# Kernel optimization log

Measured on AMD Instinct MI355X. Metric: run time of the kernel, lower is better.

The kernel has to match this reference:

```python
import jax, jax.numpy as jnp
import numpy as np

B, S, D = 4, 2048, 1024
H, N = 8, 16
HN = H * N
L = 2
DFF = 4 * D
V = 32000
C = 1024


def layer_norm(x, g, b, eps=1e-5):
    m = jnp.mean(x, axis=-1, keepdims=True)
    v = jnp.mean(jnp.square(x - m), axis=-1, keepdims=True)
    return (x - m) * jax.lax.rsqrt(v + eps) * g + b


def ssm_scan(alpha, b):
    # alpha, b: [B, S, H, N]; h_t = alpha_t * h_{t-1} + b_t
    h0 = jnp.zeros((alpha.shape[0], alpha.shape[2], alpha.shape[3]), alpha.dtype)

    def step(h, ab):
        a_t, b_t = ab
        h = a_t * h + b_t
        return h, h

    _, hs = jax.lax.scan(step, h0, (jnp.swapaxes(alpha, 0, 1), jnp.swapaxes(b, 0, 1)))
    return jnp.swapaxes(hs, 0, 1)  # [B, S, H, N]


def setup_inputs() -> dict:
    key = jax.random.key(0)
    ks = jax.random.split(key, 30)

    def rn(k, shape, std):
        return (jax.random.normal(k, shape, jnp.float32) * std).astype(jnp.float32)

    xav_d_hn = float(np.sqrt(6.0 / (D + HN)))
    xav_hn_d = float(np.sqrt(6.0 / (HN + D)))
    xav_d_ff = float(np.sqrt(6.0 / (D + DFF)))
    xav_ff_d = float(np.sqrt(6.0 / (DFF + D)))

    inp = {
        "x": jax.random.randint(ks[0], (B, S), 0, V),
        "emb": rn(ks[1], (V, D), 0.02),
        "pos_emb": rn(ks[2], (S, D), 0.02),
        # SSM layers (stacked over L). Weights stored [in, out].
        "alpha_W": rn(ks[3], (L, D, HN), 0.01),
        "alpha_b": jnp.full((L, HN), 2.0, jnp.float32),
        "in_W": jax.random.uniform(ks[4], (L, D, HN), jnp.float32, -xav_d_hn, xav_d_hn),
        "in_b": jnp.zeros((L, HN), jnp.float32),
        "out_W": jax.random.uniform(ks[5], (L, HN, D), jnp.float32, -xav_hn_d, xav_hn_d),
        "out_b": jnp.zeros((L, D), jnp.float32),
        "ssm_g": jnp.ones((L, D), jnp.float32),
        "ssm_beta": jnp.zeros((L, D), jnp.float32),
        # SwiGLU layers
        "w1_W": jax.random.uniform(ks[6], (L, D, DFF), jnp.float32, -xav_d_ff, xav_d_ff),
        "w1_b": jnp.zeros((L, DFF), jnp.float32),
        "w2_W": jax.random.uniform(ks[7], (L, DFF, D), jnp.float32, -xav_ff_d, xav_ff_d),
        "w2_b": jnp.zeros((L, D), jnp.float32),
        "w3_W": jax.random.uniform(ks[8], (L, D, DFF), jnp.float32, -xav_d_ff, xav_d_ff),
        "w3_b": jnp.zeros((L, DFF), jnp.float32),
        "ff_g": jnp.ones((L, D), jnp.float32),
        "ff_beta": jnp.zeros((L, D), jnp.float32),
        # output norm + head
        "on_g": jnp.ones((D,), jnp.float32),
        "on_beta": jnp.zeros((D,), jnp.float32),
        "h1_W": rn(ks[9], (D, 2 * D), 0.02),
        "h1_b": jnp.zeros((2 * D,), jnp.float32),
        "h2_W": rn(ks[10], (2 * D, C), 0.02),
        "h2_b": jnp.zeros((C,), jnp.float32),
    }
    return inp


def reference(x, emb, pos_emb, alpha_W, alpha_b, in_W, in_b, out_W, out_b,
              ssm_g, ssm_beta, w1_W, w1_b, w2_W, w2_b, w3_W, w3_b,
              ff_g, ff_beta, on_g, on_beta, h1_W, h1_b, h2_W, h2_b):
    b, s = x.shape
    h = emb[x] + pos_emb[:s][None, :, :]  # [B,S,D]
    for l in range(L):
        # DiagonalSSMLayer (dropout eval -> identity)
        xn = layer_norm(h, ssm_g[l], ssm_beta[l])
        alpha = jax.nn.sigmoid(xn @ alpha_W[l] + alpha_b[l]).reshape(b, s, H, N)
        bb = (xn @ in_W[l] + in_b[l]).reshape(b, s, H, N)
        hs = ssm_scan(alpha, bb).reshape(b, s, HN)
        h = h + hs @ out_W[l] + out_b[l]
        # SwiGLU block
        xn = layer_norm(h, ff_g[l], ff_beta[l])
        h = h + (jax.nn.silu(xn @ w1_W[l] + w1_b[l]) * (xn @ w3_W[l] + w3_b[l])) @ w2_W[l] + w2_b[l]
    h = layer_norm(h, on_g, on_beta)
    logits = jax.nn.gelu(h @ h1_W + h1_b, approximate=False) @ h2_W + h2_b
    return logits  # [B, S, C]
```

## Files before the change

kernel.cpp:

```cpp
#include <hip/hip_runtime.h>
#include <hip/hip_bf16.h>
#include <math.h>

#define B_    4
#define S_    2048
#define D_    1024
#define H_    8
#define N_    16
#define HN_   128
#define L_    2
#define DFF_  4096
#define C_    1024
#define MTOK  8192

using bf16 = __hip_bfloat16;
typedef __attribute__((ext_vector_type(8))) short  short8;
typedef __attribute__((ext_vector_type(4))) float  f32x4;

static __device__ __forceinline__ float sigmoidf_(float x) { return 1.f / (1.f + expf(-x)); }

static __device__ __forceinline__ unsigned short f2bf_bits(float f) {
    bf16 h = __float2bfloat16(f);
    return __builtin_bit_cast(unsigned short, h);
}

#define GLOAD_LDS(gp, lp) \
    __builtin_amdgcn_global_load_lds((__attribute__((address_space(1))) void*)(gp), \
                                     (__attribute__((address_space(3))) void*)(lp), 16, 0, 0)

#define VMCNT(n) asm volatile("s_waitcnt vmcnt(" #n ")" ::: "memory")
#define BARRIER() do { asm volatile("" ::: "memory"); __builtin_amdgcn_s_barrier(); \
                       asm volatile("" ::: "memory"); } while (0)

__global__ __launch_bounds__(256) void transpose_k(const float* __restrict__ src,
                                                   bf16* __restrict__ dst,
                                                   int K, int N, int rstride, int roff) {
    __shared__ float t[32][33];
    int n0 = blockIdx.x * 32, k0 = blockIdx.y * 32;
    int tx = threadIdx.x, ty = threadIdx.y;
    #pragma unroll
    for (int i = ty; i < 32; i += 8)
        t[i][tx] = src[(size_t)(k0 + i) * N + n0 + tx];
    __syncthreads();
    #pragma unroll
    for (int i = ty; i < 32; i += 8)
        dst[((size_t)(n0 + i) * rstride + roff) * K + k0 + tx] = __float2bfloat16(t[tx][i]);
}

__global__ __launch_bounds__(256) void embed_k(const int* __restrict__ x,
                                               const float* __restrict__ emb,
                                               const float* __restrict__ pos,
                                               float* __restrict__ h) {
    int tok = blockIdx.x, t = threadIdx.x;
    int id = x[tok];
    int s  = tok & (S_ - 1);
    float4 a = ((const float4*)(emb + (size_t)id * D_))[t];
    float4 p = ((const float4*)(pos + (size_t)s * D_))[t];
    float4 r; r.x = a.x + p.x; r.y = a.y + p.y; r.z = a.z + p.z; r.w = a.w + p.w;
    ((float4*)(h + (size_t)tok * D_))[t] = r;
}

__global__ __launch_bounds__(256) void ln_k(const float* __restrict__ x,
                                            const float* __restrict__ g,
                                            const float* __restrict__ be,
                                            bf16* __restrict__ out) {
    int row = blockIdx.x, t = threadIdx.x;
    float4 v = ((const float4*)(x + (size_t)row * D_))[t];
    float s  = v.x + v.y + v.z + v.w;
    float sq = v.x * v.x + v.y * v.y + v.z * v.z + v.w * v.w;
    #pragma unroll
    for (int o = 32; o > 0; o >>= 1) {
        s  += __shfl_down(s, o);
        sq += __shfl_down(sq, o);
    }
    __shared__ float red[8];
    __shared__ float mv[2];
    int wave = t >> 6, lane = t & 63;
    if (lane == 0) { red[wave] = s; red[4 + wave] = sq; }
    __syncthreads();
    if (t == 0) {
        float S0 = red[0] + red[1] + red[2] + red[3];
        float Q  = red[4] + red[5] + red[6] + red[7];
        float m  = S0 * (1.f / 1024.f);
        float var = Q * (1.f / 1024.f) - m * m;
        mv[0] = m; mv[1] = rsqrtf(var + 1e-5f);
    }
    __syncthreads();
    float m = mv[0], rs = mv[1];
    float4 gg = ((const float4*)g)[t];
    float4 bb = ((const float4*)be)[t];
    ushort4 o;
    o.x = f2bf_bits((v.x - m) * rs * gg.x + bb.x);
    o.y = f2bf_bits((v.y - m) * rs * gg.y + bb.y);
    o.z = f2bf_bits((v.z - m) * rs * gg.z + bb.z);
    o.w = f2bf_bits((v.w - m) * rs * gg.w + bb.w);
    ((ushort4*)(out + (size_t)row * D_))[t] = o;
}

__global__ __launch_bounds__(256) void ssm_scan_k(const float* __restrict__ ab,
                                                  bf16* __restrict__ hs) {
    const int CL = S_ / 16;
    int bh = blockIdx.x;
    int b = bh >> 3, hh = bh & 7;
    int t = threadIdx.x;
    int chunk = t >> 4, n = t & 15;
    size_t rowbase = (size_t)b * S_ + (size_t)chunk * CL;
    const float* ap = ab + rowbase * 256 + hh * 16 + n;
    const float* bp = ap + 128;

    float A = 1.f, Bc = 0.f;
    for (int i = 0; i < CL; i++) {
        float a = ap[(size_t)i * 256], bv = bp[(size_t)i * 256];
        A *= a; Bc = a * Bc + bv;
    }
    __shared__ float sA[16][16], sB[16][16], sH[16][16];
    sA[chunk][n] = A; sB[chunk][n] = Bc;
    __syncthreads();
    if (t < 16) {
        float run = 0.f;
        #pragma unroll
        for (int c = 0; c < 16; c++) {
            sH[c][t] = run;
            run = sA[c][t] * run + sB[c][t];
        }
    }
    __syncthreads();
    float hrun = sH[chunk][n];
    bf16* op = hs + rowbase * 128 + hh * 16 + n;
    for (int i = 0; i < CL; i++) {
        float a = ap[(size_t)i * 256], bv = bp[(size_t)i * 256];
        hrun = a * hrun + bv;
        op[(size_t)i * 128] = __float2bfloat16(hrun);
    }
}

enum { EP_AB = 0, EP_BIAS_RES = 1, EP_BIAS_BF16 = 2, EP_SILUMUL_BF16 = 3,
       EP_GELU_BF16 = 4, EP_BIAS_F32 = 5, EP_W13 = 6 };

template <int EP>
static __device__ __forceinline__ void ep_store(
    float v, size_t idx, int col,
    float* __restrict__ outF, bf16* __restrict__ outB,
    const float* __restrict__ b1, const float* __restrict__ b2,
    const float* __restrict__ resF, const bf16* __restrict__ resB) {
    if constexpr (EP == EP_AB) {
        if (col < HN_) v = sigmoidf_(v + b1[col]);
        else           v = v + b2[col - HN_];
        outF[idx] = v;
    } else if constexpr (EP == EP_BIAS_RES) {
        outF[idx] = v + b1[col] + resF[idx];
    } else if constexpr (EP == EP_BIAS_BF16) {
        outB[idx] = __float2bfloat16(v + b1[col]);
    } else if constexpr (EP == EP_SILUMUL_BF16) {
        float c1 = __bfloat162float(resB[idx]);
        float sil = c1 * sigmoidf_(c1);
        outB[idx] = __float2bfloat16((v + b1[col]) * sil);
    } else if constexpr (EP == EP_GELU_BF16) {
        float xv = v + b1[col];
        outB[idx] = __float2bfloat16(0.5f * xv * (1.f + erff(xv * 0.70710678118f)));
    } else {
        outF[idx] = v + b1[col];
    }
}

template <int EP>
__global__ __launch_bounds__(256) void gemm_k(
    const bf16* __restrict__ A, const bf16* __restrict__ W,
    float* __restrict__ outF, bf16* __restrict__ outB,
    const float* __restrict__ b1, const float* __restrict__ b2,
    const float* __restrict__ resF, const bf16* __restrict__ resB,
    int M, int N, int K) {
    __shared__ __align__(16) bf16 As[128 * 64];
    __shared__ __align__(16) bf16 Bs[128 * 64];
    const int tid = threadIdx.x;
    const int wave = tid >> 6, lane = tid & 63;
    const int bm = blockIdx.x * 128, bn = blockIdx.y * 128;
    const int wr = (wave >> 1) * 64, wc = (wave & 1) * 64;

    f32x4 acc[4][4];
    #pragma unroll
    for (int m = 0; m < 4; m++)
        #pragma unroll
        for (int n = 0; n < 4; n++) acc[m][n] = f32x4{0.f, 0.f, 0.f, 0.f};

    const int srow = tid >> 3;
    const int skc  = (tid & 7) * 8;

    for (int k0 = 0; k0 < K; k0 += 64) {
        #pragma unroll
        for (int rr = 0; rr < 4; rr++) {
            int row = rr * 32 + srow;
            GLOAD_LDS(A + (size_t)(bm + row) * K + k0 + skc, As + row * 64 + skc);
            GLOAD_LDS(W + (size_t)(bn + row) * K + k0 + skc, Bs + row * 64 + skc);
        }
        __syncthreads();
        #pragma unroll
        for (int ks = 0; ks < 2; ks++) {
            const int kb = ks * 32 + (lane >> 4) * 8;
            short8 af[4], bfr[4];
            #pragma unroll
            for (int m = 0; m < 4; m++)
                af[m] = *reinterpret_cast<const short8*>(As + (wr + m * 16 + (lane & 15)) * 64 + kb);
            #pragma unroll
            for (int n = 0; n < 4; n++)
                bfr[n] = *reinterpret_cast<const short8*>(Bs + (wc + n * 16 + (lane & 15)) * 64 + kb);
            #pragma unroll
            for (int m = 0; m < 4; m++)
                #pragma unroll
                for (int n = 0; n < 4; n++)
                    acc[m][n] = __builtin_amdgcn_mfma_f32_16x16x32_bf16(af[m], bfr[n], acc[m][n], 0, 0, 0);
        }
        __syncthreads();
    }

    const int cb = bn + wc + (lane & 15);
    const int rb = bm + wr + (lane >> 4) * 4;
    #pragma unroll
    for (int m = 0; m < 4; m++)
        #pragma unroll
        for (int n = 0; n < 4; n++) {
            int col = cb + n * 16;
            #pragma unroll
            for (int i = 0; i < 4; i++) {
                int row = rb + m * 16 + i;
                ep_store<EP>(acc[m][n][i], (size_t)row * N + col, col,
                             outF, outB, b1, b2, resF, resB);
            }
        }
}

extern __shared__ __align__(16) char smem_g256[];

template <int BN, int EP>
__global__ __launch_bounds__(512, 2) void gemm256_k(
    const bf16* __restrict__ A, const bf16* __restrict__ W,
    float* __restrict__ outF, bf16* __restrict__ outB,
    const float* __restrict__ b1, const float* __restrict__ b2,
    const float* __restrict__ resF, const bf16* __restrict__ resB,
    int M, int N, int K) {
    constexpr int NR   = BN / 64;
    constexpr int NBJ  = BN / 64;
    constexpr int WCS  = NR * 16;
    constexpr int ASZB = 256 * 64 * 2;
    constexpr int BSZB = BN * 64 * 2;
    constexpr int BUFB = ASZB + BSZB;

    const int tid = threadIdx.x;
    const int wid = tid >> 6, lane = tid & 63;
    const int wr = wid >> 2, wc = wid & 3;
    const int l15 = lane & 15, l4 = lane >> 4;

    const int nwg = gridDim.x;
    const int bid = ((int)blockIdx.x & 7) * (nwg >> 3) + ((int)blockIdx.x >> 3);
    const int gx = M >> 8;
    const int bm = (bid % gx) * 256;
    const int bn = (bid / gx) * BN;

    const int nt = K >> 6;

    const int tr   = tid >> 3;
    const int cc8  = (((tid & 7) ^ (tr & 7)) << 3);
    const bf16* gA0 = A + (size_t)(bm + tr) * K + cc8;
    const bf16* gB0 = W + (size_t)(bn + tr) * K + cc8;
    const int ldsc = tid << 4;

    auto stageA = [&](int t, int j) {
        GLOAD_LDS(gA0 + (size_t)j * ((size_t)K << 6) + ((size_t)t << 6),
                  smem_g256 + (size_t)(t & 1) * BUFB + ldsc + (j << 13));
    };
    auto stageB = [&](int t, int j) {
        GLOAD_LDS(gB0 + (size_t)j * ((size_t)K << 6) + ((size_t)t << 6),
                  smem_g256 + (size_t)(t & 1) * BUFB + ASZB + ldsc + (j << 13));
    };

    const int swz   = (lane & 7) << 4;
    const int kof0  = ((l4 << 4)) ^ swz;
    const int kof1  = (64 + (l4 << 4)) ^ swz;
    const int rbaseA = (wr * 128 + l15) << 7;
    const int rbaseB = ASZB + ((wc * WCS + l15) << 7);

    auto rdA = [&](int bo, int m, int kof) -> short8 {
        return *reinterpret_cast<const short8*>(smem_g256 + bo + rbaseA + (m << 11) + kof);
    };
    auto rdB = [&](int bo, int n, int kof) -> short8 {
        return *reinterpret_cast<const short8*>(smem_g256 + bo + rbaseB + (n << 11) + kof);
    };

    f32x4 acc[8][NR];
    #pragma unroll
    for (int m = 0; m < 8; m++)
        #pragma unroll
        for (int n = 0; n < NR; n++) acc[m][n] = f32x4{0.f, 0.f, 0.f, 0.f};

    #pragma unroll
    for (int j = 0; j < 4; j++) stageA(0, j);
    #pragma unroll
    for (int j = 0; j < NBJ; j++) stageB(0, j);
    #pragma unroll
    for (int j = 0; j < 4; j++) stageA(1, j);
    #pragma unroll
    for (int j = 0; j < NBJ; j++) stageB(1, j);

    short8 a0[4], a1[4], bF0[NR], bF1[NR];

    for (int v = 0; v < nt; ++v) {
        const int bo = (v & 1) * BUFB;
        if (v == 0)            { if constexpr (BN == 256) VMCNT(8); else VMCNT(6); }
        else if (v + 1 < nt)   { if constexpr (BN == 256) VMCNT(6); else VMCNT(4); }
        else                   VMCNT(0);
        BARRIER();

        #pragma unroll
        for (int m = 0; m < 4; m++) a0[m] = rdA(bo, m, kof0);
        #pragma unroll
        for (int n = 0; n < NR; n++) bF0[n] = rdB(bo, n, kof0);
        #pragma unroll
        for (int n = 0; n < NR; n++) bF1[n] = rdB(bo, n, kof1);
        if (v >= 1 && v + 1 < nt) { stageA(v + 1, 1); stageA(v + 1, 3); }
        BARRIER();
        #pragma unroll
        for (int m = 0; m < 4; m++) a1[m] = rdA(bo, m, kof1);
        __builtin_amdgcn_s_setprio(1);
        #pragma unroll
        for (int m = 0; m < 4; m++)
            #pragma unroll
            for (int n = 0; n < NR; n++)
                acc[m][n] = __builtin_amdgcn_mfma_f32_16x16x32_bf16(a0[m], bF0[n], acc[m][n], 0, 0, 0);
        __builtin_amdgcn_s_setprio(0);
        BARRIER();

        #pragma unroll
        for (int m = 0; m < 4; m++) a0[m] = rdA(bo, 4 + m, kof0);
        __builtin_amdgcn_s_setprio(1);
        #pragma unroll
        for (int m = 0; m < 4; m++)
            #pragma unroll
            for (int n = 0; n < NR; n++)
                acc[m][n] = __builtin_amdgcn_mfma_f32_16x16x32_bf16(a1[m], bF1[n], acc[m][n], 0, 0, 0);
        __builtin_amdgcn_s_setprio(0);
        BARRIER();

        if (v + 2 < nt) {
            #pragma unroll
            for (int j = 0; j < NBJ; j++) stageB(v + 2, j);
            stageA(v + 2, 0); stageA(v + 2, 2);
        }
        #pragma unroll
        for (int m = 0; m < 4; m++) a1[m] = rdA(bo, 4 + m, kof1);
        __builtin_amdgcn_s_setprio(1);
        #pragma unroll
        for (int m = 0; m < 4; m++)
            #pragma unroll
            for (int n = 0; n < NR; n++)
                acc[4 + m][n] = __builtin_amdgcn_mfma_f32_16x16x32_bf16(a0[m], bF0[n], acc[4 + m][n], 0, 0, 0);
        __builtin_amdgcn_s_setprio(0);
        BARRIER();

        __builtin_amdgcn_s_setprio(1);
        #pragma unroll
        for (int m = 0; m < 4; m++)
            #pragma unroll
            for (int n = 0; n < NR; n++)
                acc[4 + m][n] = __builtin_amdgcn_mfma_f32_16x16x32_bf16(a1[m], bF1[n], acc[4 + m][n], 0, 0, 0);
        __builtin_amdgcn_s_setprio(0);
        BARRIER();
    }

    const int gc0 = bn + wc * WCS + l15;
    const int gr0 = bm + wr * 128 + l4 * 4;
    #pragma unroll
    for (int m = 0; m < 8; m++)
        #pragma unroll
        for (int n = 0; n < NR; n++) {
            int col = gc0 + n * 16;
            #pragma unroll
            for (int i = 0; i < 4; i++) {
                int row = gr0 + m * 16 + i;
                if constexpr (EP == EP_W13) {
                    float xv = acc[m][n][i] + ((col & 1) ? b2[col >> 1] : b1[col >> 1]);
                    float part = __shfl_xor(xv, 1);
                    if (!(col & 1)) {
                        float r = xv * sigmoidf_(xv) * part;
                        outB[(size_t)row * (N >> 1) + (col >> 1)] = __float2bfloat16(r);
                    }
                } else {
                    ep_store<EP>(acc[m][n][i], (size_t)row * N + col, col,
                                 outF, outB, b1, b2, resF, resB);
                }
            }
        }
}

extern "C" void kernel_launch(void* const* d_in, const int* in_sizes, int n_in,
                              void* d_out, int out_size, void* d_ws, size_t ws_size,
                              hipStream_t stream) {
    const int*   x       = (const int*)  d_in[0];
    const float* emb     = (const float*)d_in[1];
    const float* pos_emb = (const float*)d_in[2];
    const float* alpha_W = (const float*)d_in[3];
    const float* alpha_b = (const float*)d_in[4];
    const float* in_W    = (const float*)d_in[5];
    const float* in_b    = (const float*)d_in[6];
    const float* out_W   = (const float*)d_in[7];
    const float* out_b   = (const float*)d_in[8];
    const float* ssm_g   = (const float*)d_in[9];
    const float* ssm_be  = (const float*)d_in[10];
    const float* w1_W    = (const float*)d_in[11];
    const float* w1_b    = (const float*)d_in[12];
    const float* w2_W    = (const float*)d_in[13];
    const float* w2_b    = (const float*)d_in[14];
    const float* w3_W    = (const float*)d_in[15];
    const float* w3_b    = (const float*)d_in[16];
    const float* ff_g    = (const float*)d_in[17];
    const float* ff_be   = (const float*)d_in[18];
    const float* on_g    = (const float*)d_in[19];
    const float* on_be   = (const float*)d_in[20];
    const float* h1_W    = (const float*)d_in[21];
    const float* h1_b    = (const float*)d_in[22];
    const float* h2_W    = (const float*)d_in[23];
    const float* h2_b    = (const float*)d_in[24];
    float* outp = (float*)d_out;
    (void)in_sizes; (void)n_in; (void)out_size; (void)ws_size;

    hipFuncSetAttribute((const void*)gemm256_k<256, EP_W13>,       hipFuncAttributeMaxDynamicSharedMemorySize, 131072);
    hipFuncSetAttribute((const void*)gemm256_k<256, EP_GELU_BF16>, hipFuncAttributeMaxDynamicSharedMemorySize, 131072);
    hipFuncSetAttribute((const void*)gemm256_k<128, EP_BIAS_RES>,  hipFuncAttributeMaxDynamicSharedMemorySize, 98304);
    hipFuncSetAttribute((const void*)gemm256_k<128, EP_BIAS_F32>,  hipFuncAttributeMaxDynamicSharedMemorySize, 98304);

    char* ws = (char*)d_ws;
    size_t off = 0;
    auto alloc = [&](size_t bytes) { size_t o = off; off += (bytes + 255) & ~(size_t)255; return o; };
    float* h    = (float*)(ws + alloc((size_t)MTOK * D_ * 4));
    bf16*  xn   = (bf16*) (ws + alloc((size_t)MTOK * D_ * 2));
    bf16*  abw  = (bf16*) (ws + alloc((size_t)L_ * 256 * D_ * 2));
    bf16*  outw = (bf16*) (ws + alloc((size_t)L_ * D_ * HN_ * 2));
    bf16*  wfw  = (bf16*) (ws + alloc((size_t)L_ * 2 * DFF_ * D_ * 2));
    bf16*  w2w  = (bf16*) (ws + alloc((size_t)L_ * D_ * DFF_ * 2));
    bf16*  h1w  = (bf16*) (ws + alloc((size_t)2048 * D_ * 2));
    bf16*  h2w  = (bf16*) (ws + alloc((size_t)D_ * 2048 * 2));
    float* ab   = (float*)(ws + alloc((size_t)MTOK * 256 * 4));
    bf16*  hs   = (bf16*) (ws + alloc((size_t)MTOK * HN_ * 2));
    bf16*  c1   = (bf16*) (ws + alloc((size_t)MTOK * DFF_ * 2));

    auto T = [&](const float* src, bf16* dst, int K, int N, int rs, int ro) {
        transpose_k<<<dim3(N / 32, K / 32), dim3(32, 8), 0, stream>>>(src, dst, K, N, rs, ro);
    };

    for (int l = 0; l < L_; l++) {
        T(alpha_W + (size_t)l * D_ * HN_,  abw + (size_t)l * 256 * D_,                    D_,  HN_, 1, 0);
        T(in_W    + (size_t)l * D_ * HN_,  abw + (size_t)l * 256 * D_ + (size_t)HN_ * D_, D_,  HN_, 1, 0);
        T(out_W   + (size_t)l * HN_ * D_,  outw + (size_t)l * D_ * HN_,                   HN_, D_,  1, 0);
        T(w1_W    + (size_t)l * D_ * DFF_, wfw + (size_t)l * 2 * DFF_ * D_,               D_,  DFF_, 2, 0);
        T(w3_W    + (size_t)l * D_ * DFF_, wfw + (size_t)l * 2 * DFF_ * D_,               D_,  DFF_, 2, 1);
        T(w2_W    + (size_t)l * DFF_ * D_, w2w + (size_t)l * D_ * DFF_,                   DFF_, D_, 1, 0);
    }
    T(h1_W, h1w, D_, 2048, 1, 0);
    T(h2_W, h2w, 2048, D_, 1, 0);

    embed_k<<<MTOK, 256, 0, stream>>>(x, emb, pos_emb, h);

    for (int l = 0; l < L_; l++) {
        ln_k<<<MTOK, 256, 0, stream>>>(h, ssm_g + l * D_, ssm_be + l * D_, xn);
        gemm_k<EP_AB><<<dim3(64, 2), 256, 0, stream>>>(
            xn, abw + (size_t)l * 256 * D_, ab, nullptr,
            alpha_b + l * HN_, in_b + l * HN_, nullptr, nullptr, MTOK, 256, D_);
        ssm_scan_k<<<B_ * H_, 256, 0, stream>>>(ab, hs);
        gemm_k<EP_BIAS_RES><<<dim3(64, 8), 256, 0, stream>>>(
            hs, outw + (size_t)l * D_ * HN_, h, nullptr,
            out_b + l * D_, nullptr, h, nullptr, MTOK, D_, HN_);
        ln_k<<<MTOK, 256, 0, stream>>>(h, ff_g + l * D_, ff_be + l * D_, xn);
        gemm256_k<256, EP_W13><<<dim3((MTOK / 256) * (2 * DFF_ / 256)), 512, 131072, stream>>>(
            xn, wfw + (size_t)l * 2 * DFF_ * D_, nullptr, c1,
            w1_b + l * DFF_, w3_b + l * DFF_, nullptr, nullptr, MTOK, 2 * DFF_, D_);
        gemm256_k<128, EP_BIAS_RES><<<dim3((MTOK / 256) * (D_ / 128)), 512, 98304, stream>>>(
            c1, w2w + (size_t)l * D_ * DFF_, h, nullptr,
            w2_b + l * D_, nullptr, h, nullptr, MTOK, D_, DFF_);
    }

    ln_k<<<MTOK, 256, 0, stream>>>(h, on_g, on_be, xn);
    gemm256_k<256, EP_GELU_BF16><<<dim3((MTOK / 256) * (2048 / 256)), 512, 131072, stream>>>(
        xn, h1w, nullptr, c1, h1_b, nullptr, nullptr, nullptr, MTOK, 2048, D_);
    gemm256_k<128, EP_BIAS_F32><<<dim3((MTOK / 256) * (C_ / 128)), 512, 98304, stream>>>(
        c1, h2w, outp, nullptr, h2_b, nullptr, nullptr, nullptr, MTOK, C_, 2048);
}
```

Baseline: 1.178 ms.

## Restructure gemm256 main loop into quadrant phases with split B staging

```diff
diff --git a/kernel.cpp b/kernel.cpp
--- a/kernel.cpp
+++ b/kernel.cpp
@@ -28,7 +28,9 @@
     __builtin_amdgcn_global_load_lds((__attribute__((address_space(1))) void*)(gp), \
                                      (__attribute__((address_space(3))) void*)(lp), 16, 0, 0)
 
-#define VMCNT(n) asm volatile("s_waitcnt vmcnt(" #n ")" ::: "memory")
+#define VMCNT(n)  asm volatile("s_waitcnt vmcnt(" #n ")" ::: "memory")
+#define LGKM(n)   asm volatile("s_waitcnt lgkmcnt(" #n ")" ::: "memory")
+#define SBAR()    __builtin_amdgcn_sched_barrier(0)
 #define BARRIER() do { asm volatile("" ::: "memory"); __builtin_amdgcn_s_barrier(); \
                        asm volatile("" ::: "memory"); } while (0)
 
@@ -239,11 +241,12 @@
     const float* __restrict__ resF, const bf16* __restrict__ resB,
     int M, int N, int K) {
     constexpr int NR   = BN / 64;
-    constexpr int NBJ  = BN / 64;
+    constexpr int NRH  = NR / 2;
     constexpr int WCS  = NR * 16;
     constexpr int ASZB = 256 * 64 * 2;
     constexpr int BSZB = BN * 64 * 2;
     constexpr int BUFB = ASZB + BSZB;
+    constexpr int NHSH = (BN == 256) ? 14 : 13;
 
     const int tid = threadIdx.x;
     const int wid = tid >> 6, lane = tid & 63;
@@ -261,7 +264,6 @@
     const int tr   = tid >> 3;
     const int cc8  = (((tid & 7) ^ (tr & 7)) << 3);
     const bf16* gA0 = A + (size_t)(bm + tr) * K + cc8;
-    const bf16* gB0 = W + (size_t)(bn + tr) * K + cc8;
     const int ldsc = tid << 4;
 
     auto stageA = [&](int t, int j) {
@@ -269,21 +271,26 @@
                   smem_g256 + (size_t)(t & 1) * BUFB + ldsc + (j << 13));
     };
     auto stageB = [&](int t, int j) {
-        GLOAD_LDS(gB0 + (size_t)j * ((size_t)K << 6) + ((size_t)t << 6),
+        int gbrow;
+        if constexpr (BN == 256)
+            gbrow = bn + (((j << 1) + (tr >> 5)) & 3) * 64 + ((j >> 1) << 5) + (tr & 31);
+        else
+            gbrow = bn + (((tr >> 4) & 3) << 5) + (j << 4) + (tr & 15);
+        GLOAD_LDS(W + (size_t)gbrow * K + ((size_t)t << 6) + cc8,
                   smem_g256 + (size_t)(t & 1) * BUFB + ASZB + ldsc + (j << 13));
     };
 
-    const int swz   = (lane & 7) << 4;
-    const int kof0  = ((l4 << 4)) ^ swz;
-    const int kof1  = (64 + (l4 << 4)) ^ swz;
+    const int swz  = (lane & 7) << 4;
+    const int kof0 = (l4 << 4) ^ swz;
+    const int kof1 = (64 + (l4 << 4)) ^ swz;
     const int rbaseA = (wr * 128 + l15) << 7;
-    const int rbaseB = ASZB + ((wc * WCS + l15) << 7);
-
-    auto rdA = [&](int bo, int m, int kof) -> short8 {
-        return *reinterpret_cast<const short8*>(smem_g256 + bo + rbaseA + (m << 11) + kof);
+    const int rbaseB = ASZB + ((wc * (WCS / 2) + l15) << 7);
+
+    auto rdA = [&](int bo, int mh, int m, int kof) -> short8 {
+        return *reinterpret_cast<const short8*>(smem_g256 + bo + rbaseA + (mh << 13) + (m << 11) + kof);
     };
-    auto rdB = [&](int bo, int n, int kof) -> short8 {
-        return *reinterpret_cast<const short8*>(smem_g256 + bo + rbaseB + (n << 11) + kof);
+    auto rdB = [&](int bo, int nh, int f, int kof) -> short8 {
+        return *reinterpret_cast<const short8*>(smem_g256 + bo + rbaseB + (nh << NHSH) + (f << 11) + kof);
     };
 
     f32x4 acc[8][NR];
@@ -295,75 +302,96 @@
     #pragma unroll
     for (int j = 0; j < 4; j++) stageA(0, j);
     #pragma unroll
-    for (int j = 0; j < NBJ; j++) stageB(0, j);
+    for (int j = 0; j < NR; j++) stageB(0, j);
     #pragma unroll
     for (int j = 0; j < 4; j++) stageA(1, j);
     #pragma unroll
-    for (int j = 0; j < NBJ; j++) stageB(1, j);
-
-    short8 a0[4], a1[4], bF0[NR], bF1[NR];
+    for (int j = 0; j < NRH; j++) stageB(1, j);
+
+    short8 A0[2][4], A1[2][4], Bf[2][NRH];
 
     for (int v = 0; v < nt; ++v) {
         const int bo = (v & 1) * BUFB;
-        if (v == 0)            { if constexpr (BN == 256) VMCNT(8); else VMCNT(6); }
-        else if (v + 1 < nt)   { if constexpr (BN == 256) VMCNT(6); else VMCNT(4); }
-        else                   VMCNT(0);
+        if (v + 1 < nt) { if constexpr (BN == 256) VMCNT(6); else VMCNT(5); }
+        else            VMCNT(0);
         BARRIER();
 
         #pragma unroll
-        for (int m = 0; m < 4; m++) a0[m] = rdA(bo, m, kof0);
-        #pragma unroll
-        for (int n = 0; n < NR; n++) bF0[n] = rdB(bo, n, kof0);
-        #pragma unroll
-        for (int n = 0; n < NR; n++) bF1[n] = rdB(bo, n, kof1);
-        if (v >= 1 && v + 1 < nt) { stageA(v + 1, 1); stageA(v + 1, 3); }
-        BARRIER();
-        #pragma unroll
-        for (int m = 0; m < 4; m++) a1[m] = rdA(bo, m, kof1);
+        for (int ks = 0; ks < 2; ks++) {
+            int kof = ks ? kof1 : kof0;
+            #pragma unroll
+            for (int m = 0; m < 4; m++) A0[ks][m] = rdA(bo, 0, m, kof);
+            #pragma unroll
+            for (int f = 0; f < NRH; f++) Bf[ks][f] = rdB(bo, 0, f, kof);
+        }
+        if (v + 1 < nt) {
+            #pragma unroll
+            for (int j = 0; j < NRH; j++) stageB(v + 1, NRH + j);
+        }
+        if constexpr (BN == 256) LGKM(8);
+        BARRIER(); LGKM(0); SBAR();
         __builtin_amdgcn_s_setprio(1);
         #pragma unroll
         for (int m = 0; m < 4; m++)
             #pragma unroll
-            for (int n = 0; n < NR; n++)
-                acc[m][n] = __builtin_amdgcn_mfma_f32_16x16x32_bf16(a0[m], bF0[n], acc[m][n], 0, 0, 0);
+            for (int f = 0; f < NRH; f++)
+                #pragma unroll
+                for (int ks = 0; ks < 2; ks++)
+                    acc[m][f] = __builtin_amdgcn_mfma_f32_16x16x32_bf16(A0[ks][m], Bf[ks][f], acc[m][f], 0, 0, 0);
         __builtin_amdgcn_s_setprio(0);
         BARRIER();
 
         #pragma unroll
-        for (int m = 0; m < 4; m++) a0[m] = rdA(bo, 4 + m, kof0);
+        for (int ks = 0; ks < 2; ks++) {
+            int kof = ks ? kof1 : kof0;
+            #pragma unroll
+            for (int m = 0; m < 4; m++) A1[ks][m] = rdA(bo, 1, m, kof);
+        }
+        if (v + 2 < nt) { stageA(v + 2, 0); stageA(v + 2, 2); }
+        BARRIER(); LGKM(0); SBAR();
         __builtin_amdgcn_s_setprio(1);
         #pragma unroll
         for (int m = 0; m < 4; m++)
             #pragma unroll
-            for (int n = 0; n < NR; n++)
-                acc[m][n] = __builtin_amdgcn_mfma_f32_16x16x32_bf16(a1[m], bF1[n], acc[m][n], 0, 0, 0);
+            for (int f = 0; f < NRH; f++)
+                #pragma unroll
+                for (int ks = 0; ks < 2; ks++)
+                    acc[4 + m][f] = __builtin_amdgcn_mfma_f32_16x16x32_bf16(A1[ks][m], Bf[ks][f], acc[4 + m][f], 0, 0, 0);
         __builtin_amdgcn_s_setprio(0);
         BARRIER();
 
-        if (v + 2 < nt) {
-            #pragma unroll
-            for (int j = 0; j < NBJ; j++) stageB(v + 2, j);
-            stageA(v + 2, 0); stageA(v + 2, 2);
-        }
-        #pragma unroll
-        for (int m = 0; m < 4; m++) a1[m] = rdA(bo, 4 + m, kof1);
+        #pragma unroll
+        for (int ks = 0; ks < 2; ks++) {
+            int kof = ks ? kof1 : kof0;
+            #pragma unroll
+            for (int f = 0; f < NRH; f++) Bf[ks][f] = rdB(bo, 1, f, kof);
+        }
+        if (v + 2 < nt) { stageA(v + 2, 1); stageA(v + 2, 3); }
+        BARRIER(); LGKM(0); SBAR();
         __builtin_amdgcn_s_setprio(1);
         #pragma unroll
         for (int m = 0; m < 4; m++)
             #pragma unroll
-            for (int n = 0; n < NR; n++)
-                acc[4 + m][n] = __builtin_amdgcn_mfma_f32_16x16x32_bf16(a0[m], bF0[n], acc[4 + m][n], 0, 0, 0);
+            for (int f = 0; f < NRH; f++)
+                #pragma unroll
+                for (int ks = 0; ks < 2; ks++)
+                    acc[m][NRH + f] = __builtin_amdgcn_mfma_f32_16x16x32_bf16(A0[ks][m], Bf[ks][f], acc[m][NRH + f], 0, 0, 0);
         __builtin_amdgcn_s_setprio(0);
         BARRIER();
 
+        if (v + 2 < nt) {
+            #pragma unroll
+            for (int j = 0; j < NRH; j++) stageB(v + 2, j);
+        }
         __builtin_amdgcn_s_setprio(1);
         #pragma unroll
         for (int m = 0; m < 4; m++)
             #pragma unroll
-            for (int n = 0; n < NR; n++)
-                acc[4 + m][n] = __builtin_amdgcn_mfma_f32_16x16x32_bf16(a1[m], bF1[n], acc[4 + m][n], 0, 0, 0);
+            for (int f = 0; f < NRH; f++)
+                #pragma unroll
+                for (int ks = 0; ks < 2; ks++)
+                    acc[4 + m][NRH + f] = __builtin_amdgcn_mfma_f32_16x16x32_bf16(A1[ks][m], Bf[ks][f], acc[4 + m][NRH + f], 0, 0, 0);
         __builtin_amdgcn_s_setprio(0);
-        BARRIER();
     }
 
     const int gc0 = bn + wc * WCS + l15;
```

Measured after the change: 1.197 ms. About the same (+1.6%).
